# Kernel tuning notes

Measured on AMD Instinct MI355X. Metric: run time of the kernel, lower is better.

## Reference

```python
import jax, jax.numpy as jnp
import numpy as np

DIM = 128
B, LQ, LK = 8, 2048, 2048


def setup_inputs() -> dict:
    key = jax.random.key(0)
    k1, k2, k3 = jax.random.split(key, 3)
    output = jax.random.normal(k1, (B, LQ, DIM), dtype=jnp.float32)
    context = jax.random.normal(k2, (B, LK, DIM), dtype=jnp.float32)
    mask = jax.random.randint(k3, (B, LQ, LK), 0, 2).astype(jnp.bool_)
    return {"output": output, "context": context, "mask": mask}


def reference(output, context, mask):
    temperature = jnp.asarray(np.power(DIM, 0.5), dtype=output.dtype)
    # scores: [B, Lq, Lk]
    attn = jnp.einsum('bqd,bkd->bqk', output, context) / temperature
    attn = jnp.where(mask, -jnp.inf, attn)
    out_attn = jax.nn.log_softmax(attn, axis=-1)
    p = jax.nn.softmax(attn, axis=-1)
    # dropout is identity in eval/reference mode
    out = jnp.einsum('bqk,bkd->bqd', p, context)
    return (out, out_attn)
```

## Files before the change

### kernel.cpp

```cpp
#include <hip/hip_runtime.h>
#include <cstdint>


#define DIMV 128
constexpr int BB = 8;
constexpr int LQ = 2048;
constexpr int LK = 2048;
constexpr float RTEMP = 0.08838834764831843f;

typedef _Float16 half8 __attribute__((ext_vector_type(8)));
typedef float float4v __attribute__((ext_vector_type(4)));

__global__ __launch_bounds__(256) void prep_kernel(const float* __restrict__ q,
                                                   const float* __restrict__ ctx,
                                                   const unsigned char* __restrict__ mask,
                                                   _Float16* __restrict__ Qf,
                                                   _Float16* __restrict__ Kf,
                                                   _Float16* __restrict__ Vf,
                                                   uint32_t* __restrict__ pm) {
    const int tid = threadIdx.x;
    if (blockIdx.x >= 1536) {
        const int mb = blockIdx.x - 1536;
        const int g  = mb * 8 + (tid >> 5);
        const int w0 = (tid & 31) * 2;
        const uint4* p = (const uint4*)(mask + (size_t)g * 2048 + w0 * 32);
        uint32_t* dst = pm + (size_t)g * 64 + w0;
        for (int wi = 0; wi < 2; wi++) {
            uint32_t bits = 0;
            for (int h = 0; h < 2; h++) {
                uint4 v = p[wi * 2 + h];
                uint32_t d[4] = {v.x, v.y, v.z, v.w};
                for (int k = 0; k < 4; k++) {
                    uint32_t x = d[k];
                    x |= x >> 4; x |= x >> 2; x |= x >> 1;
                    x &= 0x01010101u;
                    bits |= ((x * 0x01020408u) >> 24 & 0xF) << (h * 16 + k * 4);
                }
            }
            dst[wi] = bits;
        }
        return;
    }
    __shared__ float tile[32][132];
    const int mode = blockIdx.x >> 9;
    const int t    = blockIdx.x & 511;
    const int b    = t >> 6;
    const int r0   = (t & 63) * 32;
    const float4* s4 = (const float4*)((mode == 0 ? q : ctx) + ((size_t)b * 2048 + r0) * DIMV);
    for (int v = 0; v < 4; v++) {
        int off = tid + v * 256;
        float4 f = s4[off];
        int row = off >> 5, c4 = (off & 31) * 4;
        tile[row][c4 + 0] = f.x; tile[row][c4 + 1] = f.y;
        tile[row][c4 + 2] = f.z; tile[row][c4 + 3] = f.w;
    }
    __syncthreads();
    if (mode < 2) {
        _Float16* dst = (mode == 0 ? Qf : Kf) + (size_t)b * (2048 * DIMV);
        for (int c = 0; c < 2; c++) {
            int chunk = tid + c * 256;
            int t2 = chunk >> 8, kk = (chunk >> 6) & 3, lane = chunk & 63;
            int quad = lane >> 4, l16 = lane & 15;
            int r = t2 * 16 + l16, d0 = kk * 32 + quad * 8;
            half8 h;
            for (int e = 0; e < 8; e++) h[e] = (_Float16)tile[r][d0 + e];
            size_t tl = (size_t)(r0 >> 4) + t2;
            *(half8*)(dst + ((tl * 4 + kk) * 64 + lane) * 8) = h;
        }
    } else {
        _Float16* dst = Vf + (size_t)b * (2048 * DIMV);
        size_t i = r0 >> 5;
        for (int c = 0; c < 2; c++) {
            int chunk = tid + c * 256;
            int nt = chunk >> 6, lane = chunk & 63;
            int quad = lane >> 4, l16 = lane & 15;
            half8 h;
            for (int e = 0; e < 8; e++) h[e] = (_Float16)tile[quad * 8 + e][nt * 16 + l16];
            *(half8*)(dst + ((i * 8 + nt) * 64 + lane) * 8) = h;
        }
    }
}

__global__ __launch_bounds__(256, 4)
void attn_kernel(const uint32_t* __restrict__ pm,
                 const _Float16* __restrict__ Qf, const _Float16* __restrict__ Kf,
                 const _Float16* __restrict__ Vf,
                 float* __restrict__ out, float* __restrict__ out_attn) {
    constexpr int PSTR = 40;
    __shared__ float sumbuf[4][16];
    __shared__ float loglbuf[16];
    __shared__ float obuf[16][128];
    __shared__ __attribute__((aligned(16))) _Float16 pscr[4][16 * PSTR];

    const int tid  = threadIdx.x;
    const int wave = tid >> 6;
    const int lane = tid & 63;
    const int l16  = lane & 15;
    const int quad = lane >> 4;

    const int b  = blockIdx.x & 7;
    const int qt = blockIdx.x >> 3;
    const int q0 = qt * 16;

    const _Float16* Qb = Qf + (size_t)b * (2048 * DIMV);
    const _Float16* Kb = Kf + (size_t)b * (2048 * DIMV);
    const _Float16* Vb = Vf + (size_t)b * (2048 * DIMV);
    const uint32_t* pmb = pm + ((size_t)b * 2048 + q0) * 64;

    for (int i = tid; i < 16 * 128; i += 256) ((float*)obuf)[i] = 0.f;

    half8 afrag[4];
#pragma unroll
    for (int kk = 0; kk < 4; kk++)
        afrag[kk] = *(const half8*)(Qb + (((size_t)qt * 4 + kk) * 64 + lane) * 8);

    float lsum[4] = {0.f, 0.f, 0.f, 0.f};
    for (int ch = 0; ch < 16; ch++) {
        const int w = wave * 16 + ch;
        uint32_t mw[4];
#pragma unroll
        for (int r = 0; r < 4; r++)
            mw[r] = pmb[(size_t)(quad * 4 + r) * 64 + w];
#pragma unroll
        for (int h = 0; h < 2; h++) {
            const int cT = w * 2 + h;
            const _Float16* kp = Kb + (size_t)cT * 2048;
            float4v acc = (float4v){0.f, 0.f, 0.f, 0.f};
#pragma unroll
            for (int kk = 0; kk < 4; kk++) {
                half8 bf = *(const half8*)(kp + (kk * 64 + lane) * 8);
                acc = __builtin_amdgcn_mfma_f32_16x16x32_f16(afrag[kk], bf, acc, 0, 0, 0);
            }
            const int bitpos = h * 16 + l16;
#pragma unroll
            for (int r = 0; r < 4; r++) {
                float e = __expf(acc[r] * RTEMP);
                lsum[r] += ((mw[r] >> bitpos) & 1u) ? 0.f : e;
            }
        }
    }
#pragma unroll
    for (int r = 0; r < 4; r++) {
        float v = lsum[r];
        v += __shfl_xor(v, 1);
        v += __shfl_xor(v, 2);
        v += __shfl_xor(v, 4);
        v += __shfl_xor(v, 8);
        lsum[r] = v;
    }
    if (l16 == 0)
#pragma unroll
        for (int r = 0; r < 4; r++)
            sumbuf[wave][quad * 4 + r] = lsum[r];
    __syncthreads();
    if (tid < 16)
        loglbuf[tid] = __logf(sumbuf[0][tid] + sumbuf[1][tid] + sumbuf[2][tid] + sumbuf[3][tid]);
    __syncthreads();
    float logl[4];
#pragma unroll
    for (int r = 0; r < 4; r++) logl[r] = loglbuf[quad * 4 + r];

    _Float16* myscr = &pscr[wave][0];
    float4v oacc[8];
#pragma unroll
    for (int nt = 0; nt < 8; nt++) oacc[nt] = (float4v){0.f, 0.f, 0.f, 0.f};

    for (int ch = 0; ch < 16; ch++) {
        const int w = wave * 16 + ch;
        uint32_t mw[4];
#pragma unroll
        for (int r = 0; r < 4; r++)
            mw[r] = pmb[(size_t)(quad * 4 + r) * 64 + w];
#pragma unroll
        for (int h = 0; h < 2; h++) {
            const int cT = w * 2 + h;
            const _Float16* kp = Kb + (size_t)cT * 2048;
            float4v acc = (float4v){0.f, 0.f, 0.f, 0.f};
#pragma unroll
            for (int kk = 0; kk < 4; kk++) {
                half8 bf = *(const half8*)(kp + (kk * 64 + lane) * 8);
                acc = __builtin_amdgcn_mfma_f32_16x16x32_f16(afrag[kk], bf, acc, 0, 0, 0);
            }
            const int bitpos = h * 16 + l16;
#pragma unroll
            for (int r = 0; r < 4; r++) {
                float s = acc[r] * RTEMP;
                bool masked = (mw[r] >> bitpos) & 1u;
                float logp = masked ? -1.0e30f : (s - logl[r]);
                out_attn[((size_t)b * 2048 + q0 + quad * 4 + r) * 2048 + cT * 16 + l16] = logp;
                float p = masked ? 0.f : __expf(logp);
                myscr[(quad * 4 + r) * PSTR + h * 16 + l16] = (_Float16)p;
            }
        }
        half8 pa = *(half8*)(myscr + l16 * PSTR + quad * 8);
        const int kidx = wave * 16 + ch;
#pragma unroll
        for (int nt = 0; nt < 8; nt++) {
            half8 bf = *(const half8*)(Vb + (((size_t)kidx * 8 + nt) * 64 + lane) * 8);
            oacc[nt] = __builtin_amdgcn_mfma_f32_16x16x32_f16(pa, bf, oacc[nt], 0, 0, 0);
        }
    }

#pragma unroll
    for (int nt = 0; nt < 8; nt++)
#pragma unroll
        for (int r = 0; r < 4; r++)
            atomicAdd(&obuf[quad * 4 + r][nt * 16 + l16], oacc[nt][r]);
    __syncthreads();
    for (int i = tid; i < 16 * 128; i += 256) {
        int row = i >> 7, col = i & 127;
        out[((size_t)b * 2048 + q0 + row) * 128 + col] = obuf[row][col];
    }
}

extern "C" void kernel_launch(void* const* d_in, const int* in_sizes, int n_in,
                              void* d_out, int out_size, void* d_ws, size_t ws_size,
                              hipStream_t stream) {
    const float* q_f32 = (const float*)d_in[0];
    const float* c_f32 = (const float*)d_in[1];
    const unsigned char* mask = (const unsigned char*)d_in[2];

    float* out      = (float*)d_out;
    float* out_attn = out + (size_t)BB * LQ * DIMV;

    _Float16* Qf = (_Float16*)d_ws;
    _Float16* Kf = Qf + (size_t)BB * LQ * DIMV;
    _Float16* Vf = Kf + (size_t)BB * LK * DIMV;
    uint32_t* pm = (uint32_t*)(Vf + (size_t)BB * LK * DIMV);

    prep_kernel<<<1536 + 2048, 256, 0, stream>>>(q_f32, c_f32, mask, Qf, Kf, Vf, pm);
    attn_kernel<<<BB * (LQ / 16), 256, 0, stream>>>(pm, Qf, Kf, Vf, out, out_attn);
}
```

Measured before the change: 313.5 us.

## Use single-wave blocks covering 32 query rows with double-buffered K/V loads

The attention kernel now launches one 64-thread wave per block. Each wave handles two 16-row query tiles, so every K and V fragment is reused across two MFMA row tiles, and each wave walks all 64 key chunks itself instead of splitting keys across four waves. This removes the shared-memory atomic reduction of the output and the cross-wave log-sum reduction. K fragments are double-buffered in registers, the mask tile is staged in LDS, and the out_attn and out writes become nontemporal stores. In exchange the grid halves to 512 single-wave blocks, each doing a longer serial loop with higher register pressure, which may reduce latency hiding.

```diff
diff --git a/kernel.cpp b/kernel.cpp
--- a/kernel.cpp
+++ b/kernel.cpp
@@ -81,136 +81,177 @@
     }
 }
 
-__global__ __launch_bounds__(256, 4)
+__global__ __launch_bounds__(64)
 void attn_kernel(const uint32_t* __restrict__ pm,
                  const _Float16* __restrict__ Qf, const _Float16* __restrict__ Kf,
                  const _Float16* __restrict__ Vf,
                  float* __restrict__ out, float* __restrict__ out_attn) {
-    constexpr int PSTR = 40;
-    __shared__ float sumbuf[4][16];
-    __shared__ float loglbuf[16];
-    __shared__ float obuf[16][128];
-    __shared__ __attribute__((aligned(16))) _Float16 pscr[4][16 * PSTR];
-
-    const int tid  = threadIdx.x;
-    const int wave = tid >> 6;
-    const int lane = tid & 63;
+    constexpr int PSTR = 36;
+    __shared__ uint32_t smask[32 * 64];
+    __shared__ __attribute__((aligned(16))) _Float16 pscr[2][16 * PSTR];
+
+    const int lane = threadIdx.x;
     const int l16  = lane & 15;
     const int quad = lane >> 4;
 
     const int b  = blockIdx.x & 7;
-    const int qt = blockIdx.x >> 3;
-    const int q0 = qt * 16;
+    const int g  = blockIdx.x >> 3;
+    const int q0 = g * 32;
 
     const _Float16* Qb = Qf + (size_t)b * (2048 * DIMV);
     const _Float16* Kb = Kf + (size_t)b * (2048 * DIMV);
     const _Float16* Vb = Vf + (size_t)b * (2048 * DIMV);
     const uint32_t* pmb = pm + ((size_t)b * 2048 + q0) * 64;
 
-    for (int i = tid; i < 16 * 128; i += 256) ((float*)obuf)[i] = 0.f;
-
-    half8 afrag[4];
-#pragma unroll
-    for (int kk = 0; kk < 4; kk++)
-        afrag[kk] = *(const half8*)(Qb + (((size_t)qt * 4 + kk) * 64 + lane) * 8);
-
-    float lsum[4] = {0.f, 0.f, 0.f, 0.f};
-    for (int ch = 0; ch < 16; ch++) {
-        const int w = wave * 16 + ch;
-        uint32_t mw[4];
-#pragma unroll
-        for (int r = 0; r < 4; r++)
-            mw[r] = pmb[(size_t)(quad * 4 + r) * 64 + w];
+    for (int i = 0; i < 32; i++)
+        smask[i * 64 + lane] = pmb[(size_t)i * 64 + lane];
+
+    half8 afrag[2][4];
+#pragma unroll
+    for (int rt = 0; rt < 2; rt++)
+#pragma unroll
+        for (int kk = 0; kk < 4; kk++)
+            afrag[rt][kk] = *(const half8*)(Qb + (((size_t)(g * 2 + rt) * 4 + kk) * 64 + lane) * 8);
+
+    half8 kb0[2][4], kb1[2][4];
+
+    auto loadK = [&](half8 (&buf)[2][4], int c) {
+#pragma unroll
+        for (int h = 0; h < 2; h++)
+#pragma unroll
+            for (int kk = 0; kk < 4; kk++)
+                buf[h][kk] = *(const half8*)(Kb + (((size_t)(c * 2 + h) * 4 + kk) * 64 + lane) * 8);
+    };
+
+    float lsum[2][4];
+#pragma unroll
+    for (int rt = 0; rt < 2; rt++)
+#pragma unroll
+        for (int r = 0; r < 4; r++) lsum[rt][r] = 0.f;
+
+    auto computeA = [&](half8 (&buf)[2][4], int c) {
+        uint32_t mw[2][4];
+#pragma unroll
+        for (int rt = 0; rt < 2; rt++)
+#pragma unroll
+            for (int r = 0; r < 4; r++)
+                mw[rt][r] = smask[(rt * 16 + quad * 4 + r) * 64 + c];
 #pragma unroll
         for (int h = 0; h < 2; h++) {
-            const int cT = w * 2 + h;
-            const _Float16* kp = Kb + (size_t)cT * 2048;
-            float4v acc = (float4v){0.f, 0.f, 0.f, 0.f};
-#pragma unroll
-            for (int kk = 0; kk < 4; kk++) {
-                half8 bf = *(const half8*)(kp + (kk * 64 + lane) * 8);
-                acc = __builtin_amdgcn_mfma_f32_16x16x32_f16(afrag[kk], bf, acc, 0, 0, 0);
+            float4v acc[2];
+#pragma unroll
+            for (int rt = 0; rt < 2; rt++) {
+                acc[rt] = (float4v){0.f, 0.f, 0.f, 0.f};
+#pragma unroll
+                for (int kk = 0; kk < 4; kk++)
+                    acc[rt] = __builtin_amdgcn_mfma_f32_16x16x32_f16(afrag[rt][kk], buf[h][kk], acc[rt], 0, 0, 0);
             }
             const int bitpos = h * 16 + l16;
 #pragma unroll
-            for (int r = 0; r < 4; r++) {
-                float e = __expf(acc[r] * RTEMP);
-                lsum[r] += ((mw[r] >> bitpos) & 1u) ? 0.f : e;
-            }
-        }
-    }
-#pragma unroll
-    for (int r = 0; r < 4; r++) {
-        float v = lsum[r];
-        v += __shfl_xor(v, 1);
-        v += __shfl_xor(v, 2);
-        v += __shfl_xor(v, 4);
-        v += __shfl_xor(v, 8);
-        lsum[r] = v;
-    }
-    if (l16 == 0)
-#pragma unroll
-        for (int r = 0; r < 4; r++)
-            sumbuf[wave][quad * 4 + r] = lsum[r];
-    __syncthreads();
-    if (tid < 16)
-        loglbuf[tid] = __logf(sumbuf[0][tid] + sumbuf[1][tid] + sumbuf[2][tid] + sumbuf[3][tid]);
-    __syncthreads();
-    float logl[4];
-#pragma unroll
-    for (int r = 0; r < 4; r++) logl[r] = loglbuf[quad * 4 + r];
-
-    _Float16* myscr = &pscr[wave][0];
-    float4v oacc[8];
-#pragma unroll
-    for (int nt = 0; nt < 8; nt++) oacc[nt] = (float4v){0.f, 0.f, 0.f, 0.f};
-
-    for (int ch = 0; ch < 16; ch++) {
-        const int w = wave * 16 + ch;
-        uint32_t mw[4];
-#pragma unroll
-        for (int r = 0; r < 4; r++)
-            mw[r] = pmb[(size_t)(quad * 4 + r) * 64 + w];
+            for (int rt = 0; rt < 2; rt++)
+#pragma unroll
+                for (int r = 0; r < 4; r++) {
+                    float e = __expf(acc[rt][r] * RTEMP);
+                    lsum[rt][r] += ((mw[rt][r] >> bitpos) & 1u) ? 0.f : e;
+                }
+        }
+    };
+
+    loadK(kb0, 0);
+    for (int c = 0; c < 64; c += 2) {
+        loadK(kb1, c + 1);
+        computeA(kb0, c);
+        if (c + 2 < 64) loadK(kb0, c + 2);
+        computeA(kb1, c + 1);
+    }
+
+    float logl[2][4];
+#pragma unroll
+    for (int rt = 0; rt < 2; rt++)
+#pragma unroll
+        for (int r = 0; r < 4; r++) {
+            float v = lsum[rt][r];
+            v += __shfl_xor(v, 1);
+            v += __shfl_xor(v, 2);
+            v += __shfl_xor(v, 4);
+            v += __shfl_xor(v, 8);
+            logl[rt][r] = __logf(v);
+        }
+
+    float4v oacc[8][2];
+#pragma unroll
+    for (int nt = 0; nt < 8; nt++)
+#pragma unroll
+        for (int rt = 0; rt < 2; rt++)
+            oacc[nt][rt] = (float4v){0.f, 0.f, 0.f, 0.f};
+
+    half8 vf[8];
+    auto loadV = [&](int c) {
+#pragma unroll
+        for (int nt = 0; nt < 8; nt++)
+            vf[nt] = *(const half8*)(Vb + (((size_t)c * 8 + nt) * 64 + lane) * 8);
+    };
+
+    auto computeB = [&](half8 (&buf)[2][4], int c) {
+        uint32_t mw[2][4];
+#pragma unroll
+        for (int rt = 0; rt < 2; rt++)
+#pragma unroll
+            for (int r = 0; r < 4; r++)
+                mw[rt][r] = smask[(rt * 16 + quad * 4 + r) * 64 + c];
 #pragma unroll
         for (int h = 0; h < 2; h++) {
-            const int cT = w * 2 + h;
-            const _Float16* kp = Kb + (size_t)cT * 2048;
-            float4v acc = (float4v){0.f, 0.f, 0.f, 0.f};
-#pragma unroll
-            for (int kk = 0; kk < 4; kk++) {
-                half8 bf = *(const half8*)(kp + (kk * 64 + lane) * 8);
-                acc = __builtin_amdgcn_mfma_f32_16x16x32_f16(afrag[kk], bf, acc, 0, 0, 0);
+            float4v acc[2];
+#pragma unroll
+            for (int rt = 0; rt < 2; rt++) {
+                acc[rt] = (float4v){0.f, 0.f, 0.f, 0.f};
+#pragma unroll
+                for (int kk = 0; kk < 4; kk++)
+                    acc[rt] = __builtin_amdgcn_mfma_f32_16x16x32_f16(afrag[rt][kk], buf[h][kk], acc[rt], 0, 0, 0);
             }
             const int bitpos = h * 16 + l16;
 #pragma unroll
-            for (int r = 0; r < 4; r++) {
-                float s = acc[r] * RTEMP;
-                bool masked = (mw[r] >> bitpos) & 1u;
-                float logp = masked ? -1.0e30f : (s - logl[r]);
-                out_attn[((size_t)b * 2048 + q0 + quad * 4 + r) * 2048 + cT * 16 + l16] = logp;
-                float p = masked ? 0.f : __expf(logp);
-                myscr[(quad * 4 + r) * PSTR + h * 16 + l16] = (_Float16)p;
-            }
-        }
-        half8 pa = *(half8*)(myscr + l16 * PSTR + quad * 8);
-        const int kidx = wave * 16 + ch;
-#pragma unroll
-        for (int nt = 0; nt < 8; nt++) {
-            half8 bf = *(const half8*)(Vb + (((size_t)kidx * 8 + nt) * 64 + lane) * 8);
-            oacc[nt] = __builtin_amdgcn_mfma_f32_16x16x32_f16(pa, bf, oacc[nt], 0, 0, 0);
-        }
+            for (int rt = 0; rt < 2; rt++)
+#pragma unroll
+                for (int r = 0; r < 4; r++) {
+                    float s = acc[rt][r] * RTEMP;
+                    bool masked = (mw[rt][r] >> bitpos) & 1u;
+                    float logp = masked ? -1.0e30f : (s - logl[rt][r]);
+                    __builtin_nontemporal_store(logp,
+                        &out_attn[((size_t)b * 2048 + q0 + rt * 16 + quad * 4 + r) * 2048 + (c * 2 + h) * 16 + l16]);
+                    float p = masked ? 0.f : __expf(logp);
+                    pscr[rt][(quad * 4 + r) * PSTR + h * 16 + l16] = (_Float16)p;
+                }
+        }
+        half8 pa[2];
+#pragma unroll
+        for (int rt = 0; rt < 2; rt++)
+            pa[rt] = *(half8*)(&pscr[rt][l16 * PSTR + quad * 8]);
+#pragma unroll
+        for (int nt = 0; nt < 8; nt++)
+#pragma unroll
+            for (int rt = 0; rt < 2; rt++)
+                oacc[nt][rt] = __builtin_amdgcn_mfma_f32_16x16x32_f16(pa[rt], vf[nt], oacc[nt][rt], 0, 0, 0);
+    };
+
+    loadK(kb0, 0);
+    for (int c = 0; c < 64; c += 2) {
+        loadK(kb1, c + 1);
+        loadV(c);
+        computeB(kb0, c);
+        if (c + 2 < 64) loadK(kb0, c + 2);
+        loadV(c + 1);
+        computeB(kb1, c + 1);
     }
 
 #pragma unroll
     for (int nt = 0; nt < 8; nt++)
 #pragma unroll
-        for (int r = 0; r < 4; r++)
-            atomicAdd(&obuf[quad * 4 + r][nt * 16 + l16], oacc[nt][r]);
-    __syncthreads();
-    for (int i = tid; i < 16 * 128; i += 256) {
-        int row = i >> 7, col = i & 127;
-        out[((size_t)b * 2048 + q0 + row) * 128 + col] = obuf[row][col];
-    }
+        for (int rt = 0; rt < 2; rt++)
+#pragma unroll
+            for (int r = 0; r < 4; r++)
+                __builtin_nontemporal_store(oacc[nt][rt][r],
+                    &out[((size_t)b * 2048 + q0 + rt * 16 + quad * 4 + r) * 128 + nt * 16 + l16]);
 }
 
 extern "C" void kernel_launch(void* const* d_in, const int* in_sizes, int n_in,
@@ -229,5 +270,5 @@
     uint32_t* pm = (uint32_t*)(Vf + (size_t)BB * LK * DIMV);
 
     prep_kernel<<<1536 + 2048, 256, 0, stream>>>(q_f32, c_f32, mask, Qf, Kf, Vf, pm);
-    attn_kernel<<<BB * (LQ / 16), 256, 0, stream>>>(pm, Qf, Kf, Vf, out, out_attn);
+    attn_kernel<<<BB * (LQ / 32), 64, 0, stream>>>(pm, Qf, Kf, Vf, out, out_attn);
 }
```

Result: faster. 306.8 us (-2.1%).
